# Kernel optimization log

Hardware: AMD Instinct MI355X
Metric: run time of the kernel (lower is better)

The kernel has to match this reference:

```python
import jax, jax.numpy as jnp
import numpy as np

NEG_SLOPE = 0.01  # torch.nn.LeakyReLU default


def setup_inputs() -> dict:
    key = jax.random.key(0)
    ks = jax.random.split(key, 9)
    B, S, F1, F2, N, M, E, L = 2, 256, 512, 512, 20000, 2, 320000, 3
    x = jax.random.normal(ks[0], (B, S, F1), dtype=jnp.float32)
    nodes = jax.random.normal(ks[1], (N, M, F2), dtype=jnp.float32)
    edge_index = jax.random.randint(ks[2], (2, E), 0, N, dtype=jnp.int32)
    Wp = jax.random.normal(ks[3], (F1, F2), dtype=jnp.float32) * 0.02  # torch Linear weight [out,in]
    bp = jax.random.normal(ks[4], (F1,), dtype=jnp.float32) * 0.02
    gcn_W = jax.random.normal(ks[5], (L, S, S), dtype=jnp.float32) * 0.05  # stored as [in,out]
    gcn_b = jax.random.normal(ks[6], (L, S), dtype=jnp.float32) * 0.02
    w_bp = jax.random.normal(ks[7], (S,), dtype=jnp.float32) * 0.05
    b_bp = jax.random.normal(ks[8], (1,), dtype=jnp.float32) * 0.02
    return {"x": x, "nodes": nodes, "edge_index": edge_index, "Wp": Wp, "bp": bp,
            "gcn_W": gcn_W, "gcn_b": gcn_b, "w_bp": w_bp, "b_bp": b_bp}


def reference(x, nodes, edge_index, Wp, bp, gcn_W, gcn_b, w_bp, b_bp):
    # Eval mode: dropout layers are identity.
    N = nodes.shape[0]
    L = gcn_W.shape[0]
    proj = nodes @ Wp.T + bp                         # [N, M, F1]
    score = jnp.einsum('bsk,nmk->bsn', x, proj)      # sum over M and F1 -> [B, S, N]
    h = score.transpose(0, 2, 1)                     # beliefs [B, N, S]

    # GCN normalization with self-loops: D^{-1/2} (A + I) D^{-1/2}
    src, dst = edge_index[0], edge_index[1]
    loop = jnp.arange(N, dtype=edge_index.dtype)
    row = jnp.concatenate([src, loop])               # message sources
    col = jnp.concatenate([dst, loop])               # message targets
    deg = jnp.zeros((N,), dtype=h.dtype).at[col].add(1.0)
    dinv = deg ** -0.5                               # deg >= 1 due to self-loops
    norm = dinv[row] * dinv[col]                     # [E+N]

    for l in range(L):
        hw = h @ gcn_W[l]                            # [B, N, S]
        msg = hw[:, row, :] * norm[None, :, None]    # gather + scale
        agg = jnp.zeros_like(hw).at[:, col, :].add(msg) + gcn_b[l]
        h = jax.nn.leaky_relu(agg, NEG_SLOPE)

    # belief_projection: Linear(S, 1) then squeeze -> [B, N]
    return h @ w_bp + b_bp[0]
```

## Files before the change

kernel.cpp:

```cpp
#include <hip/hip_runtime.h>
#include <cstddef>
#include <cstdint>

#define NN 20000

typedef short frag16 __attribute__((ext_vector_type(8)));
typedef float f32x4 __attribute__((ext_vector_type(4)));

__device__ inline unsigned short f32_to_bf16(float f) {
    uint32_t u = __float_as_uint(f);
    u += 0x7FFFu + ((u >> 16) & 1u);
    return (unsigned short)(u >> 16);
}

__device__ inline float4 dec4(uint2 v) {
    float4 r;
    r.x = __uint_as_float(v.x << 16);
    r.y = __uint_as_float(v.x & 0xffff0000u);
    r.z = __uint_as_float(v.y << 16);
    r.w = __uint_as_float(v.y & 0xffff0000u);
    return r;
}

__global__ __launch_bounds__(256) void prep(
    const float* __restrict__ nodes, const float* __restrict__ x,
    const float* __restrict__ gcn_W, const float* __restrict__ bp,
    const int* __restrict__ src, const int* __restrict__ dst,
    unsigned short* __restrict__ nsum16, unsigned short* __restrict__ WT,
    float* __restrict__ Tf, float* __restrict__ cvec,
    int* __restrict__ cnt, int* __restrict__ csr, int E)
{
    __shared__ __align__(16) char shmem[8704];
    const int blk = blockIdx.x, tid = threadIdx.x;
    const int eb = (E + 255) >> 8;

    if (blk < eb) {
        int e = blk * 256 + tid;
        if (e < E) {
            int d = dst[e];
            int pos = atomicAdd(&cnt[d], 1);
            if (pos < 64) csr[(d << 6) + pos] = src[e];
        }
    } else if (blk < eb + 64) {
        float* As = (float*)shmem;
        float* Bs = As + 1024;
        int t = blk - eb;
        int b = t >> 5, rem = t & 31;
        int s0 = (rem >> 3) * 64, f0 = (rem & 7) * 64;
        const float* W1 = gcn_W;
        const float* xb = x + (size_t)b * 256 * 512;
        int kk = tid >> 4, c4 = (tid & 15) << 2;
        int tm = tid >> 4, tn = tid & 15;
        float acc[4][4] = {};
        for (int k0 = 0; k0 < 256; k0 += 16) {
            float4 av = *(const float4*)(W1 + (size_t)(k0 + kk) * 256 + s0 + c4);
            float4 bv = *(const float4*)(xb + (size_t)(k0 + kk) * 512 + f0 + c4);
            __syncthreads();
            *(float4*)&As[kk * 64 + c4] = av;
            *(float4*)&Bs[kk * 64 + c4] = bv;
            __syncthreads();
            #pragma unroll
            for (int k = 0; k < 16; ++k) {
                float a[4], bb[4];
                *(float4*)a  = *(const float4*)&As[k * 64 + (tm << 2)];
                *(float4*)bb = *(const float4*)&Bs[k * 64 + (tn << 2)];
                #pragma unroll
                for (int i = 0; i < 4; ++i)
                    #pragma unroll
                    for (int j = 0; j < 4; ++j) acc[i][j] += a[i] * bb[j];
            }
        }
        #pragma unroll
        for (int i = 0; i < 4; ++i) {
            int row = b * 256 + s0 + (tm << 2) + i;
            *(float4*)(Tf + (size_t)row * 512 + f0 + (tn << 2)) =
                make_float4(acc[i][0], acc[i][1], acc[i][2], acc[i][3]);
        }
    } else if (blk < eb + 64 + 2512) {
        int g = (blk - eb - 64) * 256 + tid;
        int n = g >> 5, c = (g & 31) << 4;
        uint4 o0, o1;
        if (n < NN) {
            const float* r0 = nodes + (size_t)n * 1024 + c;
            const float* r1 = r0 + 512;
            float4 a0 = *(const float4*)(r0 + 0),  a1 = *(const float4*)(r0 + 4);
            float4 a2 = *(const float4*)(r0 + 8),  a3 = *(const float4*)(r0 + 12);
            float4 b0 = *(const float4*)(r1 + 0),  b1 = *(const float4*)(r1 + 4);
            float4 b2 = *(const float4*)(r1 + 8),  b3 = *(const float4*)(r1 + 12);
            o0.x = ((uint32_t)f32_to_bf16(a0.y + b0.y) << 16) | f32_to_bf16(a0.x + b0.x);
            o0.y = ((uint32_t)f32_to_bf16(a0.w + b0.w) << 16) | f32_to_bf16(a0.z + b0.z);
            o0.z = ((uint32_t)f32_to_bf16(a1.y + b1.y) << 16) | f32_to_bf16(a1.x + b1.x);
            o0.w = ((uint32_t)f32_to_bf16(a1.w + b1.w) << 16) | f32_to_bf16(a1.z + b1.z);
            o1.x = ((uint32_t)f32_to_bf16(a2.y + b2.y) << 16) | f32_to_bf16(a2.x + b2.x);
            o1.y = ((uint32_t)f32_to_bf16(a2.w + b2.w) << 16) | f32_to_bf16(a2.z + b2.z);
            o1.z = ((uint32_t)f32_to_bf16(a3.y + b3.y) << 16) | f32_to_bf16(a3.x + b3.x);
            o1.w = ((uint32_t)f32_to_bf16(a3.w + b3.w) << 16) | f32_to_bf16(a3.z + b3.z);
        } else {
            o0 = make_uint4(0, 0, 0, 0); o1 = o0;
        }
        *(uint4*)(nsum16 + (size_t)n * 512 + c) = o0;
        *(uint4*)(nsum16 + (size_t)n * 512 + c + 8) = o1;
    } else if (blk < eb + 64 + 2512 + 32) {
        unsigned short (*tsh)[68] = (unsigned short(*)[68])shmem;
        int t = blk - eb - 64 - 2512;
        int l = t >> 4, rem = t & 15;
        int c0 = (rem & 3) * 64, r0 = (rem >> 2) * 64;
        const float* inp = gcn_W + (size_t)(l + 1) * 65536;
        unsigned short* outp = WT + (size_t)l * 65536;
        int tx = tid & 15, ty = tid >> 4;
        #pragma unroll
        for (int rr = 0; rr < 4; ++rr) {
            int r = ty * 4 + rr;
            float4 v = *(const float4*)(inp + (size_t)(r0 + r) * 256 + c0 + tx * 4);
            tsh[tx * 4 + 0][r] = f32_to_bf16(v.x);
            tsh[tx * 4 + 1][r] = f32_to_bf16(v.y);
            tsh[tx * 4 + 2][r] = f32_to_bf16(v.z);
            tsh[tx * 4 + 3][r] = f32_to_bf16(v.w);
        }
        __syncthreads();
        #pragma unroll
        for (int cc = 0; cc < 4; ++cc) {
            int c = ty * 4 + cc;
            ushort4 o = *(ushort4*)&tsh[c][tx * 4];
            *(ushort4*)(outp + (size_t)(c0 + c) * 256 + r0 + tx * 4) = o;
        }
    } else {
        int row = (blk - eb - 64 - 2512 - 32) * 4 + (tid >> 6);
        int lane = tid & 63;
        const float* xr = x + (size_t)row * 512;
        float s = 0.f;
        #pragma unroll
        for (int k = 0; k < 512; k += 64) s += xr[k + lane] * bp[k + lane];
        #pragma unroll
        for (int off = 32; off; off >>= 1) s += __shfl_down(s, off);
        if (lane == 0) cvec[row] = 2.0f * s;
    }
}

__global__ __launch_bounds__(256) void mid(
    const float* __restrict__ Tf, const float* __restrict__ Wp,
    const float* __restrict__ gcn_W, const float* __restrict__ cvec,
    unsigned short* __restrict__ Ub, float* __restrict__ cb2)
{
    const int blk = blockIdx.x, tid = threadIdx.x;
    if (blk >= 64) {
        int idx = (blk - 64) * 256 + tid;
        int b = idx >> 8, s = idx & 255;
        float sum = 0.f;
        for (int sp = 0; sp < 256; ++sp)
            sum += gcn_W[(size_t)sp * 256 + s] * cvec[b * 256 + sp];
        cb2[idx] = sum;
        return;
    }
    __shared__ float As[16][68];
    __shared__ float Bs[16][64];
    int bm = (blk >> 3) * 64, bn = (blk & 7) * 64;
    int arow = tid >> 2, acol = (tid & 3) << 2;
    int brow = tid >> 4, bcol = (tid & 15) << 2;
    int tm = tid >> 4, tn = tid & 15;
    float acc[4][4] = {};
    for (int k0 = 0; k0 < 512; k0 += 16) {
        float4 av = *(const float4*)(Tf + (size_t)(bm + arow) * 512 + k0 + acol);
        float4 bv = *(const float4*)(Wp + (size_t)(k0 + brow) * 512 + bn + bcol);
        __syncthreads();
        As[acol + 0][arow] = av.x; As[acol + 1][arow] = av.y;
        As[acol + 2][arow] = av.z; As[acol + 3][arow] = av.w;
        *(float4*)&Bs[brow][bcol] = bv;
        __syncthreads();
        #pragma unroll
        for (int k = 0; k < 16; ++k) {
            float a[4], b[4];
            *(float4*)a = *(const float4*)&As[k][tm << 2];
            *(float4*)b = *(const float4*)&Bs[k][tn << 2];
            #pragma unroll
            for (int i = 0; i < 4; ++i)
                #pragma unroll
                for (int j = 0; j < 4; ++j) acc[i][j] += a[i] * b[j];
        }
    }
    #pragma unroll
    for (int i = 0; i < 4; ++i) {
        int row = bm + (tm << 2) + i;
        ushort4 o;
        o.x = f32_to_bf16(acc[i][0]); o.y = f32_to_bf16(acc[i][1]);
        o.z = f32_to_bf16(acc[i][2]); o.w = f32_to_bf16(acc[i][3]);
        *(ushort4*)(Ub + (size_t)row * 512 + bn + (tn << 2)) = o;
    }
}

__global__ __launch_bounds__(256) void mgemm(
    const unsigned short* __restrict__ A, const unsigned short* __restrict__ BT,
    int K, int N, int mode,
    const float* __restrict__ cb2, const int* __restrict__ cnt,
    unsigned short* __restrict__ C)
{
    __shared__ __align__(16) unsigned short As[128 * 32];
    __shared__ __align__(16) unsigned short Bs[128 * 32];
    const int bm = blockIdx.y * 128, bn = blockIdx.x * 128;
    const int tid = threadIdx.x;
    const int lane = tid & 63, w = tid >> 6;
    const int wm = (w >> 1) << 6, wn = (w & 1) << 6;
    const int r = lane & 15, q = lane >> 4;

    f32x4 acc[4][4] = {};

    for (int k0 = 0; k0 < K; k0 += 32) {
        __syncthreads();
        #pragma unroll
        for (int t = 0; t < 2; ++t) {
            int c = t * 256 + w * 64 + lane;
            int row = c >> 2, col = (c & 3) << 3;
            __builtin_amdgcn_global_load_lds(
                (const __attribute__((address_space(1))) void*)(A + (size_t)(bm + row) * K + k0 + col),
                (__attribute__((address_space(3))) void*)(As + (size_t)(t * 256 + w * 64) * 8),
                16, 0, 0);
            __builtin_amdgcn_global_load_lds(
                (const __attribute__((address_space(1))) void*)(BT + (size_t)(bn + row) * K + k0 + col),
                (__attribute__((address_space(3))) void*)(Bs + (size_t)(t * 256 + w * 64) * 8),
                16, 0, 0);
        }
        __syncthreads();
        frag16 af[4], bf[4];
        #pragma unroll
        for (int i = 0; i < 4; ++i)
            af[i] = *(const frag16*)(As + ((wm + i * 16 + r) << 5) + (q << 3));
        #pragma unroll
        for (int j = 0; j < 4; ++j)
            bf[j] = *(const frag16*)(Bs + ((wn + j * 16 + r) << 5) + (q << 3));
        #pragma unroll
        for (int i = 0; i < 4; ++i)
            #pragma unroll
            for (int j = 0; j < 4; ++j)
                acc[i][j] = __builtin_amdgcn_mfma_f32_16x16x32_bf16(af[i], bf[j], acc[i][j], 0, 0, 0);
    }

    #pragma unroll
    for (int i = 0; i < 4; ++i) {
        #pragma unroll
        for (int rg = 0; rg < 4; ++rg) {
            int m = bm + wm + i * 16 + (q << 2) + rg;
            float sc;
            int b2 = 0, node = m;
            if (mode == 1) {
                int nc = m > NN - 1 ? NN - 1 : m;
                sc = rsqrtf((float)cnt[nc] + 1.0f);
            } else {
                b2 = m >= NN;
                node = m - b2 * NN;
                int nc = node > NN - 1 ? NN - 1 : node;
                sc = rsqrtf((float)cnt[nc] + 1.0f);
                if (node > 20095) node = 20095;
            }
            #pragma unroll
            for (int j = 0; j < 4; ++j) {
                int n = bn + wn + j * 16 + r;
                if (mode == 1) {
                    float v = (acc[i][j][rg] + cb2[n]) * sc;
                    C[(size_t)m * 512 + n] = f32_to_bf16(v);
                } else {
                    float v = acc[i][j][rg] * sc;
                    C[(size_t)node * 512 + (b2 << 8) + n] = f32_to_bf16(v);
                }
            }
        }
    }
}

__global__ __launch_bounds__(256) void aggregate_s(
    const unsigned short* __restrict__ hw, const int* __restrict__ cnt,
    const int* __restrict__ csr, const float* __restrict__ bias,
    unsigned short* __restrict__ hout,
    const float* __restrict__ w_bp, const float* __restrict__ b_bp,
    float* __restrict__ out)
{
    int n = blockIdx.x * 4 + (threadIdx.x >> 6);
    int b = blockIdx.y;
    int lane = threadIdx.x & 63;
    const unsigned short* rowp = hw + (b << 8) + (lane << 2);

    int deg = cnt[n]; if (deg > 64) deg = 64;
    int myidx = csr[(n << 6) + lane];

    float4 acc = dec4(*(const uint2*)(rowp + (size_t)n * 512));
    int e = 0;
    for (; e + 8 <= deg; e += 8) {
        int s0 = __shfl(myidx, e + 0), s1 = __shfl(myidx, e + 1);
        int s2 = __shfl(myidx, e + 2), s3 = __shfl(myidx, e + 3);
        int s4 = __shfl(myidx, e + 4), s5 = __shfl(myidx, e + 5);
        int s6 = __shfl(myidx, e + 6), s7 = __shfl(myidx, e + 7);
        uint2 u0 = *(const uint2*)(rowp + (size_t)s0 * 512);
        uint2 u1 = *(const uint2*)(rowp + (size_t)s1 * 512);
        uint2 u2 = *(const uint2*)(rowp + (size_t)s2 * 512);
        uint2 u3 = *(const uint2*)(rowp + (size_t)s3 * 512);
        uint2 u4 = *(const uint2*)(rowp + (size_t)s4 * 512);
        uint2 u5 = *(const uint2*)(rowp + (size_t)s5 * 512);
        uint2 u6 = *(const uint2*)(rowp + (size_t)s6 * 512);
        uint2 u7 = *(const uint2*)(rowp + (size_t)s7 * 512);
        float4 f0 = dec4(u0), f1 = dec4(u1), f2 = dec4(u2), f3 = dec4(u3);
        float4 f4 = dec4(u4), f5 = dec4(u5), f6 = dec4(u6), f7 = dec4(u7);
        acc.x += ((f0.x + f1.x) + (f2.x + f3.x)) + ((f4.x + f5.x) + (f6.x + f7.x));
        acc.y += ((f0.y + f1.y) + (f2.y + f3.y)) + ((f4.y + f5.y) + (f6.y + f7.y));
        acc.z += ((f0.z + f1.z) + (f2.z + f3.z)) + ((f4.z + f5.z) + (f6.z + f7.z));
        acc.w += ((f0.w + f1.w) + (f2.w + f3.w)) + ((f4.w + f5.w) + (f6.w + f7.w));
    }
    if (e + 4 <= deg) {
        int s0 = __shfl(myidx, e + 0), s1 = __shfl(myidx, e + 1);
        int s2 = __shfl(myidx, e + 2), s3 = __shfl(myidx, e + 3);
        uint2 u0 = *(const uint2*)(rowp + (size_t)s0 * 512);
        uint2 u1 = *(const uint2*)(rowp + (size_t)s1 * 512);
        uint2 u2 = *(const uint2*)(rowp + (size_t)s2 * 512);
        uint2 u3 = *(const uint2*)(rowp + (size_t)s3 * 512);
        float4 f0 = dec4(u0), f1 = dec4(u1), f2 = dec4(u2), f3 = dec4(u3);
        acc.x += (f0.x + f1.x) + (f2.x + f3.x);
        acc.y += (f0.y + f1.y) + (f2.y + f3.y);
        acc.z += (f0.z + f1.z) + (f2.z + f3.z);
        acc.w += (f0.w + f1.w) + (f2.w + f3.w);
        e += 4;
    }
    for (; e < deg; ++e) {
        int s0 = __shfl(myidx, e);
        float4 f = dec4(*(const uint2*)(rowp + (size_t)s0 * 512));
        acc.x += f.x; acc.y += f.y; acc.z += f.z; acc.w += f.w;
    }

    float dn = rsqrtf((float)deg + 1.0f);
    int s = lane << 2;
    float4 bl = *(const float4*)(bias + s);
    float4 v;
    v.x = fmaf(dn, acc.x, bl.x); v.y = fmaf(dn, acc.y, bl.y);
    v.z = fmaf(dn, acc.z, bl.z); v.w = fmaf(dn, acc.w, bl.w);
    v.x = v.x > 0.f ? v.x : 0.01f * v.x;
    v.y = v.y > 0.f ? v.y : 0.01f * v.y;
    v.z = v.z > 0.f ? v.z : 0.01f * v.z;
    v.w = v.w > 0.f ? v.w : 0.01f * v.w;

    if (out) {
        float4 w4 = *(const float4*)(w_bp + s);
        float sum = v.x * w4.x + v.y * w4.y + v.z * w4.z + v.w * w4.w;
        #pragma unroll
        for (int off = 32; off; off >>= 1) sum += __shfl_xor(sum, off);
        if (lane == 0) out[b * NN + n] = sum + b_bp[0];
    } else {
        uint2 o;
        o.x = ((uint32_t)f32_to_bf16(v.y) << 16) | f32_to_bf16(v.x);
        o.y = ((uint32_t)f32_to_bf16(v.w) << 16) | f32_to_bf16(v.z);
        *(uint2*)(hout + ((size_t)(b * NN + n)) * 256 + s) = o;
    }
}

extern "C" void kernel_launch(void* const* d_in, const int* in_sizes, int n_in,
                              void* d_out, int out_size, void* d_ws, size_t ws_size,
                              hipStream_t stream) {
    const float* x     = (const float*)d_in[0];
    const float* nodes = (const float*)d_in[1];
    const int*   eidx  = (const int*)d_in[2];
    const float* Wp    = (const float*)d_in[3];
    const float* bp    = (const float*)d_in[4];
    const float* gcn_W = (const float*)d_in[5];
    const float* gcn_b = (const float*)d_in[6];
    const float* w_bp  = (const float*)d_in[7];
    const float* b_bp  = (const float*)d_in[8];
    const int E = in_sizes[2] / 2;

    char* w = (char*)d_ws;
    auto alloc = [&](size_t bytes) { char* p = w; w += (bytes + 255) & ~(size_t)255; return p; };
    unsigned short* nsum16 = (unsigned short*)alloc((size_t)20096 * 512 * 2);
    unsigned short* hw16   = (unsigned short*)alloc((size_t)20096 * 512 * 2);
    unsigned short* hA     = (unsigned short*)alloc((size_t)40192 * 256 * 2);
    unsigned short* hB     = (unsigned short*)alloc((size_t)40192 * 256 * 2);
    float* Tf  = (float*)alloc((size_t)512 * 512 * 4);
    unsigned short* Ub = (unsigned short*)alloc((size_t)512 * 512 * 2);
    unsigned short* WT = (unsigned short*)alloc((size_t)2 * 256 * 256 * 2);
    float* cvec = (float*)alloc(512 * 4);
    float* cb2  = (float*)alloc(512 * 4);
    int*   cnt  = (int*)alloc((size_t)NN * 4);
    int*   csr  = (int*)alloc((size_t)NN * 64 * 4);

    hipMemsetAsync(cnt, 0, (size_t)NN * 4, stream);

    const int cntBlks = (E + 255) / 256;
    prep<<<cntBlks + 64 + 2512 + 32 + 128, 256, 0, stream>>>(
        nodes, x, gcn_W, bp, eidx, eidx + E, nsum16, WT, Tf, cvec, cnt, csr, E);
    mid<<<66, 256, 0, stream>>>(Tf, Wp, gcn_W, cvec, Ub, cb2);

    mgemm<<<dim3(4, 157), 256, 0, stream>>>(nsum16, Ub, 512, 512, 1, cb2, cnt, hw16);

    aggregate_s<<<dim3(5000, 2), 256, 0, stream>>>(hw16, cnt, csr, gcn_b + 0, hA,
                                                   w_bp, b_bp, nullptr);
    mgemm<<<dim3(2, 313), 256, 0, stream>>>(hA, WT, 256, 256, 2, nullptr, cnt, hw16);
    aggregate_s<<<dim3(5000, 2), 256, 0, stream>>>(hw16, cnt, csr, gcn_b + 256, hB,
                                                   w_bp, b_bp, nullptr);
    mgemm<<<dim3(2, 313), 256, 0, stream>>>(hB, WT + 65536, 256, 256, 2, nullptr, cnt, hw16);
    aggregate_s<<<dim3(5000, 2), 256, 0, stream>>>(hw16, cnt, csr, gcn_b + 512, nullptr,
                                                   w_bp, b_bp, (float*)d_out);
}
```

Baseline: 377.3 us.

## Merge batch dimension in aggregation, widen gathers, prefetch GEMM tiles, reorder prep blocks

The aggregation kernel now handles both batch entries in one wavefront. Each lane loads 16 bytes (8 bf16) per neighbour row instead of 8, so the CSR index load, degree read and shuffles are shared across batches and half as many blocks launch. The small fp32 GEMMs in prep and mid register-prefetch the next k-tile before computing the current one. The prep block order is rearranged so the atomic CSR-building blocks run last, after the dense work. This relies on the hw16 layout being [n][b*256+s] with 512 contiguous bf16 per node, and raises register use per lane.

```diff
diff --git a/kernel.cpp b/kernel.cpp
--- a/kernel.cpp
+++ b/kernel.cpp
@@ -20,6 +20,17 @@
     r.z = __uint_as_float(v.y << 16);
     r.w = __uint_as_float(v.y & 0xffff0000u);
     return r;
+}
+
+__device__ inline void dec8_add(uint4 v, float* a) {
+    a[0] += __uint_as_float(v.x << 16);
+    a[1] += __uint_as_float(v.x & 0xffff0000u);
+    a[2] += __uint_as_float(v.y << 16);
+    a[3] += __uint_as_float(v.y & 0xffff0000u);
+    a[4] += __uint_as_float(v.z << 16);
+    a[5] += __uint_as_float(v.z & 0xffff0000u);
+    a[6] += __uint_as_float(v.w << 16);
+    a[7] += __uint_as_float(v.w & 0xffff0000u);
 }
 
 __global__ __launch_bounds__(256) void prep(
@@ -32,19 +43,11 @@
 {
     __shared__ __align__(16) char shmem[8704];
     const int blk = blockIdx.x, tid = threadIdx.x;
-    const int eb = (E + 255) >> 8;
-
-    if (blk < eb) {
-        int e = blk * 256 + tid;
-        if (e < E) {
-            int d = dst[e];
-            int pos = atomicAdd(&cnt[d], 1);
-            if (pos < 64) csr[(d << 6) + pos] = src[e];
-        }
-    } else if (blk < eb + 64) {
+
+    if (blk < 64) {
         float* As = (float*)shmem;
         float* Bs = As + 1024;
-        int t = blk - eb;
+        int t = blk;
         int b = t >> 5, rem = t & 31;
         int s0 = (rem >> 3) * 64, f0 = (rem & 7) * 64;
         const float* W1 = gcn_W;
@@ -52,13 +55,17 @@
         int kk = tid >> 4, c4 = (tid & 15) << 2;
         int tm = tid >> 4, tn = tid & 15;
         float acc[4][4] = {};
+        float4 av = *(const float4*)(W1 + (size_t)kk * 256 + s0 + c4);
+        float4 bv = *(const float4*)(xb + (size_t)kk * 512 + f0 + c4);
         for (int k0 = 0; k0 < 256; k0 += 16) {
-            float4 av = *(const float4*)(W1 + (size_t)(k0 + kk) * 256 + s0 + c4);
-            float4 bv = *(const float4*)(xb + (size_t)(k0 + kk) * 512 + f0 + c4);
             __syncthreads();
             *(float4*)&As[kk * 64 + c4] = av;
             *(float4*)&Bs[kk * 64 + c4] = bv;
             __syncthreads();
+            if (k0 + 16 < 256) {
+                av = *(const float4*)(W1 + (size_t)(k0 + 16 + kk) * 256 + s0 + c4);
+                bv = *(const float4*)(xb + (size_t)(k0 + 16 + kk) * 512 + f0 + c4);
+            }
             #pragma unroll
             for (int k = 0; k < 16; ++k) {
                 float a[4], bb[4];
@@ -76,8 +83,42 @@
             *(float4*)(Tf + (size_t)row * 512 + f0 + (tn << 2)) =
                 make_float4(acc[i][0], acc[i][1], acc[i][2], acc[i][3]);
         }
-    } else if (blk < eb + 64 + 2512) {
-        int g = (blk - eb - 64) * 256 + tid;
+    } else if (blk < 96) {
+        unsigned short (*tsh)[68] = (unsigned short(*)[68])shmem;
+        int t = blk - 64;
+        int l = t >> 4, rem = t & 15;
+        int c0 = (rem & 3) * 64, r0 = (rem >> 2) * 64;
+        const float* inp = gcn_W + (size_t)(l + 1) * 65536;
+        unsigned short* outp = WT + (size_t)l * 65536;
+        int tx = tid & 15, ty = tid >> 4;
+        #pragma unroll
+        for (int rr = 0; rr < 4; ++rr) {
+            int r = ty * 4 + rr;
+            float4 v = *(const float4*)(inp + (size_t)(r0 + r) * 256 + c0 + tx * 4);
+            tsh[tx * 4 + 0][r] = f32_to_bf16(v.x);
+            tsh[tx * 4 + 1][r] = f32_to_bf16(v.y);
+            tsh[tx * 4 + 2][r] = f32_to_bf16(v.z);
+            tsh[tx * 4 + 3][r] = f32_to_bf16(v.w);
+        }
+        __syncthreads();
+        #pragma unroll
+        for (int cc = 0; cc < 4; ++cc) {
+            int c = ty * 4 + cc;
+            ushort4 o = *(ushort4*)&tsh[c][tx * 4];
+            *(ushort4*)(outp + (size_t)(c0 + c) * 256 + r0 + tx * 4) = o;
+        }
+    } else if (blk < 224) {
+        int row = (blk - 96) * 4 + (tid >> 6);
+        int lane = tid & 63;
+        const float* xr = x + (size_t)row * 512;
+        float s = 0.f;
+        #pragma unroll
+        for (int k = 0; k < 512; k += 64) s += xr[k + lane] * bp[k + lane];
+        #pragma unroll
+        for (int off = 32; off; off >>= 1) s += __shfl_down(s, off);
+        if (lane == 0) cvec[row] = 2.0f * s;
+    } else if (blk < 224 + 2512) {
+        int g = (blk - 224) * 256 + tid;
         int n = g >> 5, c = (g & 31) << 4;
         uint4 o0, o1;
         if (n < NN) {
@@ -100,40 +141,13 @@
         }
         *(uint4*)(nsum16 + (size_t)n * 512 + c) = o0;
         *(uint4*)(nsum16 + (size_t)n * 512 + c + 8) = o1;
-    } else if (blk < eb + 64 + 2512 + 32) {
-        unsigned short (*tsh)[68] = (unsigned short(*)[68])shmem;
-        int t = blk - eb - 64 - 2512;
-        int l = t >> 4, rem = t & 15;
-        int c0 = (rem & 3) * 64, r0 = (rem >> 2) * 64;
-        const float* inp = gcn_W + (size_t)(l + 1) * 65536;
-        unsigned short* outp = WT + (size_t)l * 65536;
-        int tx = tid & 15, ty = tid >> 4;
-        #pragma unroll
-        for (int rr = 0; rr < 4; ++rr) {
-            int r = ty * 4 + rr;
-            float4 v = *(const float4*)(inp + (size_t)(r0 + r) * 256 + c0 + tx * 4);
-            tsh[tx * 4 + 0][r] = f32_to_bf16(v.x);
-            tsh[tx * 4 + 1][r] = f32_to_bf16(v.y);
-            tsh[tx * 4 + 2][r] = f32_to_bf16(v.z);
-            tsh[tx * 4 + 3][r] = f32_to_bf16(v.w);
-        }
-        __syncthreads();
-        #pragma unroll
-        for (int cc = 0; cc < 4; ++cc) {
-            int c = ty * 4 + cc;
-            ushort4 o = *(ushort4*)&tsh[c][tx * 4];
-            *(ushort4*)(outp + (size_t)(c0 + c) * 256 + r0 + tx * 4) = o;
-        }
     } else {
-        int row = (blk - eb - 64 - 2512 - 32) * 4 + (tid >> 6);
-        int lane = tid & 63;
-        const float* xr = x + (size_t)row * 512;
-        float s = 0.f;
-        #pragma unroll
-        for (int k = 0; k < 512; k += 64) s += xr[k + lane] * bp[k + lane];
-        #pragma unroll
-        for (int off = 32; off; off >>= 1) s += __shfl_down(s, off);
-        if (lane == 0) cvec[row] = 2.0f * s;
+        int e = (blk - 2736) * 256 + tid;
+        if (e < E) {
+            int d = dst[e];
+            int pos = atomicAdd(&cnt[d], 1);
+            if (pos < 64) csr[(d << 6) + pos] = src[e];
+        }
     }
 }
 
@@ -159,14 +173,18 @@
     int brow = tid >> 4, bcol = (tid & 15) << 2;
     int tm = tid >> 4, tn = tid & 15;
     float acc[4][4] = {};
+    float4 av = *(const float4*)(Tf + (size_t)(bm + arow) * 512 + acol);
+    float4 bv = *(const float4*)(Wp + (size_t)brow * 512 + bn + bcol);
     for (int k0 = 0; k0 < 512; k0 += 16) {
-        float4 av = *(const float4*)(Tf + (size_t)(bm + arow) * 512 + k0 + acol);
-        float4 bv = *(const float4*)(Wp + (size_t)(k0 + brow) * 512 + bn + bcol);
         __syncthreads();
         As[acol + 0][arow] = av.x; As[acol + 1][arow] = av.y;
         As[acol + 2][arow] = av.z; As[acol + 3][arow] = av.w;
         *(float4*)&Bs[brow][bcol] = bv;
         __syncthreads();
+        if (k0 + 16 < 512) {
+            av = *(const float4*)(Tf + (size_t)(bm + arow) * 512 + k0 + 16 + acol);
+            bv = *(const float4*)(Wp + (size_t)(k0 + 16 + brow) * 512 + bn + bcol);
+        }
         #pragma unroll
         for (int k = 0; k < 16; ++k) {
             float a[4], b[4];
@@ -274,77 +292,76 @@
     float* __restrict__ out)
 {
     int n = blockIdx.x * 4 + (threadIdx.x >> 6);
-    int b = blockIdx.y;
     int lane = threadIdx.x & 63;
-    const unsigned short* rowp = hw + (b << 8) + (lane << 2);
+    const unsigned short* rowp = hw + (lane << 3);
 
     int deg = cnt[n]; if (deg > 64) deg = 64;
     int myidx = csr[(n << 6) + lane];
 
-    float4 acc = dec4(*(const uint2*)(rowp + (size_t)n * 512));
+    float acc[8] = {};
+    dec8_add(*(const uint4*)(rowp + (size_t)n * 512), acc);
     int e = 0;
     for (; e + 8 <= deg; e += 8) {
         int s0 = __shfl(myidx, e + 0), s1 = __shfl(myidx, e + 1);
         int s2 = __shfl(myidx, e + 2), s3 = __shfl(myidx, e + 3);
         int s4 = __shfl(myidx, e + 4), s5 = __shfl(myidx, e + 5);
         int s6 = __shfl(myidx, e + 6), s7 = __shfl(myidx, e + 7);
-        uint2 u0 = *(const uint2*)(rowp + (size_t)s0 * 512);
-        uint2 u1 = *(const uint2*)(rowp + (size_t)s1 * 512);
-        uint2 u2 = *(const uint2*)(rowp + (size_t)s2 * 512);
-        uint2 u3 = *(const uint2*)(rowp + (size_t)s3 * 512);
-        uint2 u4 = *(const uint2*)(rowp + (size_t)s4 * 512);
-        uint2 u5 = *(const uint2*)(rowp + (size_t)s5 * 512);
-        uint2 u6 = *(const uint2*)(rowp + (size_t)s6 * 512);
-        uint2 u7 = *(const uint2*)(rowp + (size_t)s7 * 512);
-        float4 f0 = dec4(u0), f1 = dec4(u1), f2 = dec4(u2), f3 = dec4(u3);
-        float4 f4 = dec4(u4), f5 = dec4(u5), f6 = dec4(u6), f7 = dec4(u7);
-        acc.x += ((f0.x + f1.x) + (f2.x + f3.x)) + ((f4.x + f5.x) + (f6.x + f7.x));
-        acc.y += ((f0.y + f1.y) + (f2.y + f3.y)) + ((f4.y + f5.y) + (f6.y + f7.y));
-        acc.z += ((f0.z + f1.z) + (f2.z + f3.z)) + ((f4.z + f5.z) + (f6.z + f7.z));
-        acc.w += ((f0.w + f1.w) + (f2.w + f3.w)) + ((f4.w + f5.w) + (f6.w + f7.w));
+        uint4 u0 = *(const uint4*)(rowp + (size_t)s0 * 512);
+        uint4 u1 = *(const uint4*)(rowp + (size_t)s1 * 512);
+        uint4 u2 = *(const uint4*)(rowp + (size_t)s2 * 512);
+        uint4 u3 = *(const uint4*)(rowp + (size_t)s3 * 512);
+        uint4 u4 = *(const uint4*)(rowp + (size_t)s4 * 512);
+        uint4 u5 = *(const uint4*)(rowp + (size_t)s5 * 512);
+        uint4 u6 = *(const uint4*)(rowp + (size_t)s6 * 512);
+        uint4 u7 = *(const uint4*)(rowp + (size_t)s7 * 512);
+        dec8_add(u0, acc); dec8_add(u1, acc); dec8_add(u2, acc); dec8_add(u3, acc);
+        dec8_add(u4, acc); dec8_add(u5, acc); dec8_add(u6, acc); dec8_add(u7, acc);
     }
     if (e + 4 <= deg) {
         int s0 = __shfl(myidx, e + 0), s1 = __shfl(myidx, e + 1);
         int s2 = __shfl(myidx, e + 2), s3 = __shfl(myidx, e + 3);
-        uint2 u0 = *(const uint2*)(rowp + (size_t)s0 * 512);
-        uint2 u1 = *(const uint2*)(rowp + (size_t)s1 * 512);
-        uint2 u2 = *(const uint2*)(rowp + (size_t)s2 * 512);
-        uint2 u3 = *(const uint2*)(rowp + (size_t)s3 * 512);
-        float4 f0 = dec4(u0), f1 = dec4(u1), f2 = dec4(u2), f3 = dec4(u3);
-        acc.x += (f0.x + f1.x) + (f2.x + f3.x);
-        acc.y += (f0.y + f1.y) + (f2.y + f3.y);
-        acc.z += (f0.z + f1.z) + (f2.z + f3.z);
-        acc.w += (f0.w + f1.w) + (f2.w + f3.w);
+        uint4 u0 = *(const uint4*)(rowp + (size_t)s0 * 512);
+        uint4 u1 = *(const uint4*)(rowp + (size_t)s1 * 512);
+        uint4 u2 = *(const uint4*)(rowp + (size_t)s2 * 512);
+        uint4 u3 = *(const uint4*)(rowp + (size_t)s3 * 512);
+        dec8_add(u0, acc); dec8_add(u1, acc); dec8_add(u2, acc); dec8_add(u3, acc);
         e += 4;
     }
     for (; e < deg; ++e) {
         int s0 = __shfl(myidx, e);
-        float4 f = dec4(*(const uint2*)(rowp + (size_t)s0 * 512));
-        acc.x += f.x; acc.y += f.y; acc.z += f.z; acc.w += f.w;
+        dec8_add(*(const uint4*)(rowp + (size_t)s0 * 512), acc);
     }
 
     float dn = rsqrtf((float)deg + 1.0f);
-    int s = lane << 2;
-    float4 bl = *(const float4*)(bias + s);
-    float4 v;
-    v.x = fmaf(dn, acc.x, bl.x); v.y = fmaf(dn, acc.y, bl.y);
-    v.z = fmaf(dn, acc.z, bl.z); v.w = fmaf(dn, acc.w, bl.w);
-    v.x = v.x > 0.f ? v.x : 0.01f * v.x;
-    v.y = v.y > 0.f ? v.y : 0.01f * v.y;
-    v.z = v.z > 0.f ? v.z : 0.01f * v.z;
-    v.w = v.w > 0.f ? v.w : 0.01f * v.w;
+    int b = lane >> 5;
+    int sc = (lane & 31) << 3;
+    float bl[8];
+    *(float4*)&bl[0] = *(const float4*)(bias + sc);
+    *(float4*)&bl[4] = *(const float4*)(bias + sc + 4);
+    float v[8];
+    #pragma unroll
+    for (int j = 0; j < 8; ++j) {
+        v[j] = fmaf(dn, acc[j], bl[j]);
+        v[j] = v[j] > 0.f ? v[j] : 0.01f * v[j];
+    }
 
     if (out) {
-        float4 w4 = *(const float4*)(w_bp + s);
-        float sum = v.x * w4.x + v.y * w4.y + v.z * w4.z + v.w * w4.w;
-        #pragma unroll
-        for (int off = 32; off; off >>= 1) sum += __shfl_xor(sum, off);
-        if (lane == 0) out[b * NN + n] = sum + b_bp[0];
+        float w[8];
+        *(float4*)&w[0] = *(const float4*)(w_bp + sc);
+        *(float4*)&w[4] = *(const float4*)(w_bp + sc + 4);
+        float sum = 0.f;
+        #pragma unroll
+        for (int j = 0; j < 8; ++j) sum += v[j] * w[j];
+        #pragma unroll
+        for (int off = 16; off; off >>= 1) sum += __shfl_xor(sum, off);
+        if ((lane & 31) == 0) out[b * NN + n] = sum + b_bp[0];
     } else {
-        uint2 o;
-        o.x = ((uint32_t)f32_to_bf16(v.y) << 16) | f32_to_bf16(v.x);
-        o.y = ((uint32_t)f32_to_bf16(v.w) << 16) | f32_to_bf16(v.z);
-        *(uint2*)(hout + ((size_t)(b * NN + n)) * 256 + s) = o;
+        uint4 o;
+        o.x = ((uint32_t)f32_to_bf16(v[1]) << 16) | f32_to_bf16(v[0]);
+        o.y = ((uint32_t)f32_to_bf16(v[3]) << 16) | f32_to_bf16(v[2]);
+        o.z = ((uint32_t)f32_to_bf16(v[5]) << 16) | f32_to_bf16(v[4]);
+        o.w = ((uint32_t)f32_to_bf16(v[7]) << 16) | f32_to_bf16(v[6]);
+        *(uint4*)(hout + ((size_t)(b * NN + n)) * 256 + sc) = o;
     }
 }
 
@@ -385,12 +402,12 @@
 
     mgemm<<<dim3(4, 157), 256, 0, stream>>>(nsum16, Ub, 512, 512, 1, cb2, cnt, hw16);
 
-    aggregate_s<<<dim3(5000, 2), 256, 0, stream>>>(hw16, cnt, csr, gcn_b + 0, hA,
-                                                   w_bp, b_bp, nullptr);
+    aggregate_s<<<5000, 256, 0, stream>>>(hw16, cnt, csr, gcn_b + 0, hA,
+                                          w_bp, b_bp, nullptr);
     mgemm<<<dim3(2, 313), 256, 0, stream>>>(hA, WT, 256, 256, 2, nullptr, cnt, hw16);
-    aggregate_s<<<dim3(5000, 2), 256, 0, stream>>>(hw16, cnt, csr, gcn_b + 256, hB,
-                                                   w_bp, b_bp, nullptr);
+    aggregate_s<<<5000, 256, 0, stream>>>(hw16, cnt, csr, gcn_b + 256, hB,
+                                          w_bp, b_bp, nullptr);
     mgemm<<<dim3(2, 313), 256, 0, stream>>>(hB, WT + 65536, 256, 256, 2, nullptr, cnt, hw16);
-    aggregate_s<<<dim3(5000, 2), 256, 0, stream>>>(hw16, cnt, csr, gcn_b + 512, nullptr,
-                                                   w_bp, b_bp, (float*)d_out);
-}
+    aggregate_s<<<5000, 256, 0, stream>>>(hw16, cnt, csr, gcn_b + 512, nullptr,
+                                          w_bp, b_bp, (float*)d_out);
+}
```

After: 378.2 us. No clear change (+0.2%).
